# Performance work log

Hardware: AMD Instinct MI355X
Metric: run time of the kernel (lower is better)

## Reference

```python
import jax, jax.numpy as jnp
import numpy as np

T = 1.0  # softmax temperature (module default t=1.0, learn_t=False)


def setup_inputs() -> dict:
    key = jax.random.key(0)
    k1, k2 = jax.random.split(key)
    B, N, D = 8, 512, 128
    x = jax.random.normal(k1, (B, N, D), dtype=jnp.float32)
    count = jax.random.randint(k2, (B,), 0, N, dtype=jnp.int64)
    mask = jnp.ones((B, N), dtype=jnp.float32)
    return {"x": x, "count": count, "mask": mask}


def reference(x, count, mask):
    # x: [B, N, D]. count and mask are accepted but unused (as in the torch module).
    B, N, D = x.shape
    # Per-node outer products x_n x_n^T, flattened: [B, N, D*D]
    wj = jnp.einsum('bni,bnj->bnij', x, x).reshape(B, N, D * D)
    # Softmax over the node dim N, weighted sum -> second-order pooled features
    sf = jnp.sum(jax.nn.softmax(wj * T, axis=1) * wj, axis=1)  # [B, D*D]
    return sf
```

## Files before the change

kernel.cpp:

```cpp
#include <hip/hip_runtime.h>

#define BB 8
#define NN 512
#define DD 128
#define NP (NN + 4)

#define LOG2E 1.4426950408889634f
#define LN2   0.6931471805599453f

typedef float f32x2 __attribute__((ext_vector_type(2)));
union F4 { float4 v; f32x2 p[2]; };

__global__ __launch_bounds__(256) void sop_one(const float* __restrict__ x,
                                               float* __restrict__ out) {
    int bid = blockIdx.x;
    int jt = bid & 7;
    int it = (bid >> 3) & 7;
    int b  = bid >> 6;
    int i0 = it * 16, j0 = jt * 16;

    __shared__ float xi[16][NP];
    __shared__ float xj[16][NP];

    const float* xb = x + (size_t)b * NN * DD;
    int tid = threadIdx.x;

    for (int k = 0; k < 8; ++k) {
        int idx = (k << 8) + tid;
        int dq = idx & 3;
        int n  = idx >> 2;
        int d  = dq << 2;
        F4 vi, vj;
        vi.v = *(const float4*)&xb[n * DD + i0 + d];
        vj.v = *(const float4*)&xb[n * DD + j0 + d];
        xi[d + 0][n] = vi.v.x * LOG2E;
        xi[d + 1][n] = vi.v.y * LOG2E;
        xi[d + 2][n] = vi.v.z * LOG2E;
        xi[d + 3][n] = vi.v.w * LOG2E;
        xj[d + 0][n] = vj.v.x;
        xj[d + 1][n] = vj.v.y;
        xj[d + 2][n] = vj.v.z;
        xj[d + 3][n] = vj.v.w;
    }
    __syncthreads();

    int tj = tid & 15, ti = tid >> 4;
    const float* xir = xi[ti];
    const float* xjr = xj[tj];

    f32x2 s2 = {0.f, 0.f};
    f32x2 w2 = {0.f, 0.f};
    for (int n = 0; n < NN; n += 8) {
        F4 a0, c0, a1, c1;
        a0.v = *(const float4*)&xir[n];
        c0.v = *(const float4*)&xjr[n];
        a1.v = *(const float4*)&xir[n + 4];
        c1.v = *(const float4*)&xjr[n + 4];
#define PKSTEP(av, cv) { \
        f32x2 ww = (av) * (cv);                        \
        f32x2 ee = { __builtin_amdgcn_exp2f(ww.x),     \
                     __builtin_amdgcn_exp2f(ww.y) };                     \
        s2 += ee;                                      \
        w2 = __builtin_elementwise_fma(ee, ww, w2);    }
        PKSTEP(a0.p[0], c0.p[0])
        PKSTEP(a0.p[1], c0.p[1])
        PKSTEP(a1.p[0], c1.p[0])
        PKSTEP(a1.p[1], c1.p[1])
#undef PKSTEP
    }

    float s = s2.x + s2.y;
    float w = w2.x + w2.y;
    out[((size_t)b * DD + i0 + ti) * DD + j0 + tj] = w * LN2 / s;
}

extern "C" void kernel_launch(void* const* d_in, const int* in_sizes, int n_in,
                              void* d_out, int out_size, void* d_ws, size_t ws_size,
                              hipStream_t stream) {
    const float* x = (const float*)d_in[0];
    float* out = (float*)d_out;
    (void)in_sizes; (void)n_in; (void)d_ws; (void)ws_size; (void)out_size;

    sop_one<<<dim3(BB * 8 * 8), dim3(256), 0, stream>>>(x, out);
}
```

Measured before the change: 16.35 us.

## Exploit output symmetry with 8x8 upper-triangular tiles and split-N reduction

Launches one block per upper-triangular 8x8 tile pair, so only about half of the D×D entries are computed, and writes each result to both (i,j) and (j,i). Each block splits the N=512 reduction across four waves, which combine their partial sums through shared memory. This roughly halves the exp2/FMA work and keeps more blocks in flight, at the cost of an extra sync, some idle waves during the final reduction, and transposed writes that are strided rather than coalesced.

```diff
diff --git a/kernel.cpp b/kernel.cpp
--- a/kernel.cpp
+++ b/kernel.cpp
@@ -3,6 +3,9 @@
 #define BB 8
 #define NN 512
 #define DD 128
+#define SUB 8
+#define NSUB (DD / SUB)
+#define NPAIRQ (NSUB * (NSUB + 1) / 2)
 #define NP (NN + 4)
 
 #define LOG2E 1.4426950408889634f
@@ -11,24 +14,29 @@
 typedef float f32x2 __attribute__((ext_vector_type(2)));
 union F4 { float4 v; f32x2 p[2]; };
 
-__global__ __launch_bounds__(256) void sop_one(const float* __restrict__ x,
+__global__ __launch_bounds__(256) void sop_sym(const float* __restrict__ x,
                                                float* __restrict__ out) {
     int bid = blockIdx.x;
-    int jt = bid & 7;
-    int it = (bid >> 3) & 7;
-    int b  = bid >> 6;
-    int i0 = it * 16, j0 = jt * 16;
+    int q = bid % NPAIRQ;
+    int b = bid / NPAIRQ;
+    int a = (int)((sqrtf(8.0f * q + 1.0f) - 1.0f) * 0.5f);
+    while ((a + 1) * (a + 2) / 2 <= q) ++a;
+    while (a * (a + 1) / 2 > q) --a;
+    int c = q - a * (a + 1) / 2;
+    int i0 = c * SUB;
+    int j0 = a * SUB;
 
-    __shared__ float xi[16][NP];
-    __shared__ float xj[16][NP];
+    __shared__ float xi[SUB][NP];
+    __shared__ float xj[SUB][NP];
+    __shared__ f32x2 sm[3][64];
 
     const float* xb = x + (size_t)b * NN * DD;
     int tid = threadIdx.x;
 
-    for (int k = 0; k < 8; ++k) {
+    for (int k = 0; k < 4; ++k) {
         int idx = (k << 8) + tid;
-        int dq = idx & 3;
-        int n  = idx >> 2;
+        int dq = idx & 1;
+        int n  = idx >> 1;
         int d  = dq << 2;
         F4 vi, vj;
         vi.v = *(const float4*)&xb[n * DD + i0 + d];
@@ -44,13 +52,18 @@
     }
     __syncthreads();
 
-    int tj = tid & 15, ti = tid >> 4;
-    const float* xir = xi[ti];
-    const float* xjr = xj[tj];
+    int w  = tid >> 6;
+    int l  = tid & 63;
+    int r  = l >> 3;
+    int cc = l & 7;
+    const float* xir = xi[r];
+    const float* xjr = xj[cc];
 
+    int nbeg = w << 7;
     f32x2 s2 = {0.f, 0.f};
     f32x2 w2 = {0.f, 0.f};
-    for (int n = 0; n < NN; n += 8) {
+#pragma unroll 4
+    for (int n = nbeg; n < nbeg + 128; n += 8) {
         F4 a0, c0, a1, c1;
         a0.v = *(const float4*)&xir[n];
         c0.v = *(const float4*)&xjr[n];
@@ -69,9 +82,20 @@
 #undef PKSTEP
     }
 
-    float s = s2.x + s2.y;
-    float w = w2.x + w2.y;
-    out[((size_t)b * DD + i0 + ti) * DD + j0 + tj] = w * LN2 / s;
+    f32x2 part;
+    part.x = s2.x + s2.y;
+    part.y = w2.x + w2.y;
+    if (w > 0) sm[w - 1][l] = part;
+    __syncthreads();
+    if (w == 0) {
+        f32x2 p1 = sm[0][l], p2 = sm[1][l], p3 = sm[2][l];
+        float s  = ((part.x + p1.x) + (p2.x + p3.x));
+        float ww = ((part.y + p1.y) + (p2.y + p3.y));
+        float v = ww * LN2 / s;
+        int i = i0 + r, j = j0 + cc;
+        out[((size_t)b * DD + i) * DD + j] = v;
+        out[((size_t)b * DD + j) * DD + i] = v;
+    }
 }
 
 extern "C" void kernel_launch(void* const* d_in, const int* in_sizes, int n_in,
@@ -81,5 +105,5 @@
     float* out = (float*)d_out;
     (void)in_sizes; (void)n_in; (void)d_ws; (void)ws_size; (void)out_size;
 
-    sop_one<<<dim3(BB * 8 * 8), dim3(256), 0, stream>>>(x, out);
+    sop_sym<<<dim3(BB * NPAIRQ), dim3(256), 0, stream>>>(x, out);
 }
```

After: 13.44 us. -17.8%, faster.
